# Performance work log

Hardware: AMD Instinct MI355X
Metric: run time of the kernel (lower is better)

Reference implementation:

```python
import jax, jax.numpy as jnp
import numpy as np

N_NODES = 100000
N_EDGES = 1600000
IN_C, HID_C, OUT_C = 64, 64, 16


def _sage_conv(x, src, dst, W_l, b_l, W_r, num_nodes):
    # PyG SAGEConv (aggr='mean'): out = lin_l(mean_{j->i} x_j) + lin_r(x_i)
    # aggregate first (cheap small-d features), then one GEMM
    msg_sum = jax.ops.segment_sum(x[src], dst, num_segments=num_nodes)
    deg = jax.ops.segment_sum(jnp.ones_like(dst, dtype=x.dtype), dst,
                              num_segments=num_nodes)
    mean = msg_sum / jnp.maximum(deg, 1.0)[:, None]
    return mean @ W_l + b_l + x @ W_r


def setup_inputs() -> dict:
    key = jax.random.key(0)
    ks = jax.random.split(key, 8)
    x = jax.random.normal(ks[0], (N_NODES, IN_C), dtype=jnp.float32)
    edge_index = jax.random.randint(ks[1], (2, N_EDGES), 0, N_NODES, dtype=jnp.int64)
    # Glorot-ish init for weights; lin_l has bias, lin_r has none (PyG default)
    def glorot(k, fan_in, fan_out):
        s = jnp.sqrt(6.0 / (fan_in + fan_out))
        return jax.random.uniform(k, (fan_in, fan_out), jnp.float32, -s, s)
    return {
        "x": x,
        "edge_index": edge_index,
        "W1_l": glorot(ks[2], IN_C, HID_C),
        "b1": jnp.zeros((HID_C,), jnp.float32),
        "W1_r": glorot(ks[3], IN_C, HID_C),
        "W2_l": glorot(ks[4], HID_C, OUT_C),
        "b2": jnp.zeros((OUT_C,), jnp.float32),
        "W2_r": glorot(ks[5], HID_C, OUT_C),
    }


def reference(x, edge_index, W1_l, b1, W1_r, W2_l, b2, W2_r):
    src, dst = edge_index[0], edge_index[1]
    h = _sage_conv(x, src, dst, W1_l, b1, W1_r, N_NODES)
    h = jax.nn.relu(h)
    # dropout p=0.3 is identity in eval mode
    out = _sage_conv(h, src, dst, W2_l, b2, W2_r, N_NODES)
    return out
```

## Files before the change

kernel.cpp:

```cpp
#include <hip/hip_runtime.h>
#include <hip/hip_fp16.h>

#define N_NODES 100000
#define N_EDGES 1600000
#define IN_C 64
#define HID_C 64
#define OUT_C 16

#define BKT 256
#define BSH 8
#define NBKT 391
#define CAP 5120
#define GB 512
#define EPB 3125
#define G1B 1563

typedef _Float16 f16x8 __attribute__((ext_vector_type(8)));
typedef float f32x4 __attribute__((ext_vector_type(4)));
typedef float f32x16 __attribute__((ext_vector_type(16)));

__global__ __launch_bounds__(256) void k_merged1(
    const int* __restrict__ src, const int* __restrict__ dst,
    int* __restrict__ gcnt, int* __restrict__ binned,
    const float* __restrict__ x, const float* __restrict__ Wl,
    const float* __restrict__ Wr, const float* __restrict__ b,
    __half* __restrict__ p, __half* __restrict__ q) {
  __shared__ _Float16 sA[64 * 68];
  __shared__ _Float16 sW[128 * 68];
  int t = threadIdx.x;

  if (blockIdx.x < GB) {
    int* h   = (int*)sA;
    int* cur = (int*)sW;
    for (int i = t; i < NBKT; i += 256) h[i] = 0;
    __syncthreads();
    int base = blockIdx.x * EPB;
    int end = base + EPB;
    for (int e = base + t; e < end; e += 256)
      atomicAdd(&h[dst[e] >> BSH], 1);
    __syncthreads();
    for (int i = t; i < NBKT; i += 256) {
      int c = h[i];
      int b0 = atomicAdd(&gcnt[i], c);
      cur[i] = i * CAP + b0;
    }
    __syncthreads();
    for (int e = base + t; e < end; e += 256) {
      int d = dst[e];
      int pos = atomicAdd(&cur[d >> BSH], 1);
      binned[pos] = (src[e] << BSH) | (d & (BKT - 1));
    }
    return;
  }

  int n0 = (blockIdx.x - GB) * 64;

  for (int f = t; f < 1024; f += 256) {
    int r = f >> 4, c4 = f & 15;
    int n = n0 + r;
    float4 v = {0.0f, 0.0f, 0.0f, 0.0f};
    if (n < N_NODES) v = *(const float4*)&x[(size_t)n * 64 + c4 * 4];
    union { _Float16 h[4]; float2 f2; } u;
    u.h[0] = (_Float16)v.x; u.h[1] = (_Float16)v.y;
    u.h[2] = (_Float16)v.z; u.h[3] = (_Float16)v.w;
    *(float2*)&sA[r * 68 + c4 * 4] = u.f2;
  }
  for (int f = t; f < 2048; f += 256) {
    int k = f >> 5, c4 = f & 31;
    float4 w = (c4 < 16) ? *(const float4*)&Wl[k * 64 + c4 * 4]
                         : *(const float4*)&Wr[k * 64 + (c4 - 16) * 4];
    int c = c4 * 4;
    sW[(c + 0) * 68 + k] = (_Float16)w.x;
    sW[(c + 1) * 68 + k] = (_Float16)w.y;
    sW[(c + 2) * 68 + k] = (_Float16)w.z;
    sW[(c + 3) * 68 + k] = (_Float16)w.w;
  }
  __syncthreads();

  int w = t >> 6, lane = t & 63;
  int m = lane & 31, half = lane >> 5;
  int rt = w & 1, cg = w >> 1;

  f32x16 acc[2];
#pragma unroll
  for (int r = 0; r < 16; ++r) { acc[0][r] = 0.0f; acc[1][r] = 0.0f; }

  const _Float16* pA = &sA[(rt * 32 + m) * 68 + half * 8];
  const _Float16* pB0 = &sW[(cg * 64 + m) * 68 + half * 8];
  const _Float16* pB1 = &sW[(cg * 64 + 32 + m) * 68 + half * 8];
#pragma unroll
  for (int kc = 0; kc < 4; ++kc) {
    union { f16x8 v; float2 f2[2]; } a, b0, b1;
    a.f2[0] = *(const float2*)(pA + kc * 16);
    a.f2[1] = *(const float2*)(pA + kc * 16 + 4);
    b0.f2[0] = *(const float2*)(pB0 + kc * 16);
    b0.f2[1] = *(const float2*)(pB0 + kc * 16 + 4);
    b1.f2[0] = *(const float2*)(pB1 + kc * 16);
    b1.f2[1] = *(const float2*)(pB1 + kc * 16 + 4);
    acc[0] = __builtin_amdgcn_mfma_f32_32x32x16_f16(a.v, b0.v, acc[0], 0, 0, 0);
    acc[1] = __builtin_amdgcn_mfma_f32_32x32x16_f16(a.v, b1.v, acc[1], 0, 0, 0);
  }

  if (cg == 0) {
#pragma unroll
    for (int tt = 0; tt < 2; ++tt) {
      int col = tt * 32 + m;
#pragma unroll
      for (int r = 0; r < 16; ++r) {
        int row = (r & 3) + 4 * half + 8 * (r >> 2);
        int n = n0 + rt * 32 + row;
        if (n < N_NODES) p[(size_t)n * 64 + col] = __float2half(acc[tt][r]);
      }
    }
  } else {
    float bias[2] = {b[m], b[32 + m]};
#pragma unroll
    for (int tt = 0; tt < 2; ++tt) {
      int col = tt * 32 + m;
#pragma unroll
      for (int r = 0; r < 16; ++r) {
        int row = (r & 3) + 4 * half + 8 * (r >> 2);
        int n = n0 + rt * 32 + row;
        if (n < N_NODES)
          q[(size_t)n * 64 + col] = __float2half(acc[tt][r] + bias[tt]);
      }
    }
  }
}

__global__ __launch_bounds__(1024) void k_fuse1c(
    const float4* __restrict__ p1, const int* __restrict__ gcnt,
    const int* __restrict__ binned, const float* __restrict__ W2l,
    const float* __restrict__ W2r, const float* __restrict__ b2,
    const float4* __restrict__ q1, int* __restrict__ csr,
    int* __restrict__ rowstart, int* __restrict__ cnt,
    __half* __restrict__ p2, float* __restrict__ q2) {
  __shared__ int hcnt[BKT];
  __shared__ int hscan[BKT];
  __shared__ int cur[BKT];
  __shared__ int lcsr[CAP];
  __shared__ _Float16 sH[256 * 68];
  __shared__ _Float16 sW[32 * 68];
  int b = blockIdx.x;
  int t = threadIdx.x;

  if (t < 512) {
    int k = t >> 3, c4v = t & 7;
    float4 w = (c4v < 4) ? *(const float4*)&W2l[k * 16 + c4v * 4]
                         : *(const float4*)&W2r[k * 16 + (c4v - 4) * 4];
    int c = c4v * 4;
    sW[(c + 0) * 68 + k] = (_Float16)w.x;
    sW[(c + 1) * 68 + k] = (_Float16)w.y;
    sW[(c + 2) * 68 + k] = (_Float16)w.z;
    sW[(c + 3) * 68 + k] = (_Float16)w.w;
  }
  if (t < BKT) hcnt[t] = 0;
  __syncthreads();

  int start = b * CAP;
  int total = gcnt[b];
  for (int i = t; i < total; i += 1024)
    atomicAdd(&hcnt[binned[start + i] & (BKT - 1)], 1);
  __syncthreads();
  int v = 0;
  if (t < BKT) {
    v = hcnt[t];
    hscan[t] = v;
  }
  __syncthreads();
  for (int st = 1; st < 256; st <<= 1) {
    int a = 0;
    if (t < BKT && t >= st) a = hscan[t - st];
    __syncthreads();
    if (t < BKT) hscan[t] += a;
    __syncthreads();
  }
  if (t < BKT) {
    cur[t] = hscan[t] - v;
    int n = (b << BSH) + t;
    if (n < N_NODES) {
      rowstart[n] = start + hscan[t] - v;
      cnt[n] = v;
    }
  }
  __syncthreads();
  for (int i = t; i < total; i += 1024) {
    int vv = binned[start + i];
    int pos = atomicAdd(&cur[vv & (BKT - 1)], 1);
    lcsr[pos] = vv >> BSH;
  }
  __syncthreads();
  for (int i = t; i < total; i += 1024) csr[start + i] = lcsr[i];

  int g = t >> 3, c4 = t & 7;
  for (int r = g; r < BKT; r += 128) {
    int n = (b << BSH) + r;
    if (n >= N_NODES) continue;
    int deg = hcnt[r];
    int row = hscan[r] - deg;
    float acc[8];
#pragma unroll
    for (int m = 0; m < 8; ++m) acc[m] = 0.0f;
    int j = 0;
    for (; j + 8 <= deg; j += 8) {
      int idx[8];
#pragma unroll
      for (int u = 0; u < 8; ++u) idx[u] = lcsr[row + j + u];
      float4 av[8];
#pragma unroll
      for (int u = 0; u < 8; ++u) av[u] = p1[idx[u] * 8 + c4];
#pragma unroll
      for (int u = 0; u < 8; ++u) {
        const __half2* h = (const __half2*)&av[u];
#pragma unroll
        for (int m = 0; m < 4; ++m) {
          float2 f = __half22float2(h[m]);
          acc[2 * m] += f.x;
          acc[2 * m + 1] += f.y;
        }
      }
    }
    for (; j < deg; ++j) {
      float4 a = p1[lcsr[row + j] * 8 + c4];
      const __half2* h = (const __half2*)&a;
#pragma unroll
      for (int m = 0; m < 4; ++m) {
        float2 f = __half22float2(h[m]);
        acc[2 * m] += f.x;
        acc[2 * m + 1] += f.y;
      }
    }
    float inv = 1.0f / fmaxf((float)deg, 1.0f);
    float4 qv = q1[n * 8 + c4];
    __half2* qh = (__half2*)&qv;
    union { __half2 h2[2]; float2 f2; } u01, u23;
#pragma unroll
    for (int m = 0; m < 2; ++m) {
      float2 f = __half22float2(qh[m]);
      float2 s;
      s.x = fmaxf(acc[2 * m] * inv + f.x, 0.0f);
      s.y = fmaxf(acc[2 * m + 1] * inv + f.y, 0.0f);
      u01.h2[m] = __float22half2_rn(s);
    }
#pragma unroll
    for (int m = 2; m < 4; ++m) {
      float2 f = __half22float2(qh[m]);
      float2 s;
      s.x = fmaxf(acc[2 * m] * inv + f.x, 0.0f);
      s.y = fmaxf(acc[2 * m + 1] * inv + f.y, 0.0f);
      u23.h2[m - 2] = __float22half2_rn(s);
    }
    *(float2*)&sH[r * 68 + c4 * 8] = u01.f2;
    *(float2*)&sH[r * 68 + c4 * 8 + 4] = u23.f2;
  }
  __syncthreads();

  int wv = t >> 6, lane = t & 63;
  int n16 = lane & 15, quad = lane >> 4;
  f32x4 aP, aQ;
#pragma unroll
  for (int r = 0; r < 4; ++r) { aP[r] = 0.0f; aQ[r] = 0.0f; }
  const _Float16* pA = &sH[(wv * 16 + n16) * 68 + quad * 8];
  const _Float16* pBP = &sW[n16 * 68 + quad * 8];
  const _Float16* pBQ = &sW[(16 + n16) * 68 + quad * 8];
#pragma unroll
  for (int kc = 0; kc < 2; ++kc) {
    union { f16x8 v; float2 f2[2]; } a, bp, bq;
    a.f2[0] = *(const float2*)(pA + kc * 32);
    a.f2[1] = *(const float2*)(pA + kc * 32 + 4);
    bp.f2[0] = *(const float2*)(pBP + kc * 32);
    bp.f2[1] = *(const float2*)(pBP + kc * 32 + 4);
    bq.f2[0] = *(const float2*)(pBQ + kc * 32);
    bq.f2[1] = *(const float2*)(pBQ + kc * 32 + 4);
    aP = __builtin_amdgcn_mfma_f32_16x16x32_f16(a.v, bp.v, aP, 0, 0, 0);
    aQ = __builtin_amdgcn_mfma_f32_16x16x32_f16(a.v, bq.v, aQ, 0, 0, 0);
  }
  float bias = b2[n16];
#pragma unroll
  for (int r = 0; r < 4; ++r) {
    int row = wv * 16 + quad * 4 + r;
    int n = (b << BSH) + row;
    if (n < N_NODES) {
      p2[(size_t)n * 16 + n16] = __float2half(aP[r]);
      q2[(size_t)n * 16 + n16] = aQ[r] + bias;
    }
  }
}

__global__ __launch_bounds__(256) void k_fuse2(
    const float4* __restrict__ p2, const float4* __restrict__ q2,
    const int* __restrict__ rowstart, const int* __restrict__ cnt,
    const int* __restrict__ csr, float4* __restrict__ out) {
  int t = threadIdx.x;
  int n = blockIdx.x * 128 + (t >> 1);
  if (n >= N_NODES) return;
  int c8 = t & 1;
  int row = rowstart[n];
  int deg = cnt[n];
  float acc[8];
#pragma unroll
  for (int m = 0; m < 8; ++m) acc[m] = 0.0f;
  int j = 0;
  for (; j + 8 <= deg; j += 8) {
    int idx[8];
#pragma unroll
    for (int u = 0; u < 8; ++u) idx[u] = csr[row + j + u];
    float4 av[8];
#pragma unroll
    for (int u = 0; u < 8; ++u) av[u] = p2[idx[u] * 2 + c8];
#pragma unroll
    for (int u = 0; u < 8; ++u) {
      const __half2* h = (const __half2*)&av[u];
#pragma unroll
      for (int m = 0; m < 4; ++m) {
        float2 f = __half22float2(h[m]);
        acc[2 * m] += f.x;
        acc[2 * m + 1] += f.y;
      }
    }
  }
  for (; j < deg; ++j) {
    float4 a = p2[csr[row + j] * 2 + c8];
    const __half2* h = (const __half2*)&a;
#pragma unroll
    for (int m = 0; m < 4; ++m) {
      float2 f = __half22float2(h[m]);
      acc[2 * m] += f.x;
      acc[2 * m + 1] += f.y;
    }
  }
  float inv = 1.0f / fmaxf((float)deg, 1.0f);
  float4 q0 = q2[n * 4 + c8 * 2];
  float4 q1v = q2[n * 4 + c8 * 2 + 1];
  float4 o0 = {acc[0] * inv + q0.x, acc[1] * inv + q0.y,
               acc[2] * inv + q0.z, acc[3] * inv + q0.w};
  float4 o1 = {acc[4] * inv + q1v.x, acc[5] * inv + q1v.y,
               acc[6] * inv + q1v.z, acc[7] * inv + q1v.w};
  out[n * 4 + c8 * 2] = o0;
  out[n * 4 + c8 * 2 + 1] = o1;
}

extern "C" void kernel_launch(void* const* d_in, const int* in_sizes, int n_in,
                              void* d_out, int out_size, void* d_ws, size_t ws_size,
                              hipStream_t stream) {
  const float* x   = (const float*)d_in[0];
  const int* edge  = (const int*)d_in[1];
  const int* src   = edge;
  const int* dst   = edge + N_EDGES;
  const float* W1l = (const float*)d_in[2];
  const float* b1  = (const float*)d_in[3];
  const float* W1r = (const float*)d_in[4];
  const float* W2l = (const float*)d_in[5];
  const float* b2  = (const float*)d_in[6];
  const float* W2r = (const float*)d_in[7];
  float* out = (float*)d_out;

  int* gcnt     = (int*)d_ws;
  int* rowstart = gcnt + 512;
  int* cnt      = rowstart + N_NODES;
  int* binned   = cnt + N_NODES;
  int* csr      = binned + NBKT * CAP;
  __half* p1    = (__half*)(csr + NBKT * CAP);
  __half* q1    = p1 + (size_t)N_NODES * 64;
  __half* p2    = q1 + (size_t)N_NODES * 64;
  float* q2     = (float*)(p2 + (size_t)N_NODES * 16);

  hipMemsetAsync(gcnt, 0, NBKT * sizeof(int), stream);

  k_merged1<<<GB + G1B, 256, 0, stream>>>(src, dst, gcnt, binned,
                                          x, W1l, W1r, b1, p1, q1);
  k_fuse1c<<<NBKT, 1024, 0, stream>>>((const float4*)p1, gcnt, binned,
                                      W2l, W2r, b2, (const float4*)q1,
                                      csr, rowstart, cnt, p2, q2);
  k_fuse2<<<(N_NODES + 127) / 128, 256, 0, stream>>>((const float4*)p2,
                                                     (const float4*)q2,
                                                     rowstart, cnt, csr,
                                                     (float4*)out);
}
```

Measured before the change: 189.0 us.

## Halve bucket size to double fuse1c blocks and split MFMA work across waves

Shrinks destination buckets from 256 to 128 nodes, which doubles the number of k_fuse1c blocks so the 256 CUs have more work. Each thread now aggregates exactly one row, and the P and Q GEMM halves go to different waves instead of one wave doing both. The binning phase preloads src/dst into registers once instead of reading dst twice, and skips global atomics for empty buckets. The cost is more global bucket atomics and per-block setup overhead, plus tighter per-bucket capacity margins (CAP 2560).

```diff
diff --git a/kernel.cpp b/kernel.cpp
--- a/kernel.cpp
+++ b/kernel.cpp
@@ -7,12 +7,13 @@
 #define HID_C 64
 #define OUT_C 16
 
-#define BKT 256
-#define BSH 8
-#define NBKT 391
-#define CAP 5120
+#define BKT 128
+#define BSH 7
+#define NBKT 782
+#define CAP 2560
 #define GB 512
 #define EPB 3125
+#define NIT 13
 #define G1B 1563
 
 typedef _Float16 f16x8 __attribute__((ext_vector_type(8)));
@@ -36,19 +37,31 @@
     __syncthreads();
     int base = blockIdx.x * EPB;
     int end = base + EPB;
-    for (int e = base + t; e < end; e += 256)
-      atomicAdd(&h[dst[e] >> BSH], 1);
+    int dv[NIT], sv[NIT];
+#pragma unroll
+    for (int it = 0; it < NIT; ++it) {
+      int e = base + t + it * 256;
+      bool ok = (e < end);
+      dv[it] = ok ? dst[e] : -1;
+      sv[it] = ok ? src[e] : 0;
+    }
+#pragma unroll
+    for (int it = 0; it < NIT; ++it)
+      if (dv[it] >= 0) atomicAdd(&h[dv[it] >> BSH], 1);
     __syncthreads();
     for (int i = t; i < NBKT; i += 256) {
       int c = h[i];
-      int b0 = atomicAdd(&gcnt[i], c);
+      int b0 = (c > 0) ? atomicAdd(&gcnt[i], c) : 0;
       cur[i] = i * CAP + b0;
     }
     __syncthreads();
-    for (int e = base + t; e < end; e += 256) {
-      int d = dst[e];
-      int pos = atomicAdd(&cur[d >> BSH], 1);
-      binned[pos] = (src[e] << BSH) | (d & (BKT - 1));
+#pragma unroll
+    for (int it = 0; it < NIT; ++it) {
+      if (dv[it] >= 0) {
+        int d = dv[it];
+        int pos = atomicAdd(&cur[d >> BSH], 1);
+        binned[pos] = (sv[it] << BSH) | (d & (BKT - 1));
+      }
     }
     return;
   }
@@ -139,7 +152,7 @@
   __shared__ int hscan[BKT];
   __shared__ int cur[BKT];
   __shared__ int lcsr[CAP];
-  __shared__ _Float16 sH[256 * 68];
+  __shared__ _Float16 sH[128 * 68];
   __shared__ _Float16 sW[32 * 68];
   int b = blockIdx.x;
   int t = threadIdx.x;
@@ -168,7 +181,7 @@
     hscan[t] = v;
   }
   __syncthreads();
-  for (int st = 1; st < 256; st <<= 1) {
+  for (int st = 1; st < BKT; st <<= 1) {
     int a = 0;
     if (t < BKT && t >= st) a = hscan[t - st];
     __syncthreads();
@@ -192,26 +205,37 @@
   __syncthreads();
   for (int i = t; i < total; i += 1024) csr[start + i] = lcsr[i];
 
-  int g = t >> 3, c4 = t & 7;
-  for (int r = g; r < BKT; r += 128) {
+  {
+    int r = t >> 3, c4 = t & 7;
     int n = (b << BSH) + r;
-    if (n >= N_NODES) continue;
-    int deg = hcnt[r];
-    int row = hscan[r] - deg;
-    float acc[8];
-#pragma unroll
-    for (int m = 0; m < 8; ++m) acc[m] = 0.0f;
-    int j = 0;
-    for (; j + 8 <= deg; j += 8) {
-      int idx[8];
-#pragma unroll
-      for (int u = 0; u < 8; ++u) idx[u] = lcsr[row + j + u];
-      float4 av[8];
-#pragma unroll
-      for (int u = 0; u < 8; ++u) av[u] = p1[idx[u] * 8 + c4];
-#pragma unroll
-      for (int u = 0; u < 8; ++u) {
-        const __half2* h = (const __half2*)&av[u];
+    if (n < N_NODES) {
+      int deg = hcnt[r];
+      int row = hscan[r] - deg;
+      float acc[8];
+#pragma unroll
+      for (int m = 0; m < 8; ++m) acc[m] = 0.0f;
+      int j = 0;
+      for (; j + 8 <= deg; j += 8) {
+        int idx[8];
+#pragma unroll
+        for (int u = 0; u < 8; ++u) idx[u] = lcsr[row + j + u];
+        float4 av[8];
+#pragma unroll
+        for (int u = 0; u < 8; ++u) av[u] = p1[idx[u] * 8 + c4];
+#pragma unroll
+        for (int u = 0; u < 8; ++u) {
+          const __half2* h = (const __half2*)&av[u];
+#pragma unroll
+          for (int m = 0; m < 4; ++m) {
+            float2 f = __half22float2(h[m]);
+            acc[2 * m] += f.x;
+            acc[2 * m + 1] += f.y;
+          }
+        }
+      }
+      for (; j < deg; ++j) {
+        float4 a = p1[lcsr[row + j] * 8 + c4];
+        const __half2* h = (const __half2*)&a;
 #pragma unroll
         for (int m = 0; m < 4; ++m) {
           float2 f = __half22float2(h[m]);
@@ -219,70 +243,67 @@
           acc[2 * m + 1] += f.y;
         }
       }
-    }
-    for (; j < deg; ++j) {
-      float4 a = p1[lcsr[row + j] * 8 + c4];
-      const __half2* h = (const __half2*)&a;
-#pragma unroll
-      for (int m = 0; m < 4; ++m) {
-        float2 f = __half22float2(h[m]);
-        acc[2 * m] += f.x;
-        acc[2 * m + 1] += f.y;
-      }
-    }
-    float inv = 1.0f / fmaxf((float)deg, 1.0f);
-    float4 qv = q1[n * 8 + c4];
-    __half2* qh = (__half2*)&qv;
-    union { __half2 h2[2]; float2 f2; } u01, u23;
-#pragma unroll
-    for (int m = 0; m < 2; ++m) {
-      float2 f = __half22float2(qh[m]);
-      float2 s;
-      s.x = fmaxf(acc[2 * m] * inv + f.x, 0.0f);
-      s.y = fmaxf(acc[2 * m + 1] * inv + f.y, 0.0f);
-      u01.h2[m] = __float22half2_rn(s);
-    }
-#pragma unroll
-    for (int m = 2; m < 4; ++m) {
-      float2 f = __half22float2(qh[m]);
-      float2 s;
-      s.x = fmaxf(acc[2 * m] * inv + f.x, 0.0f);
-      s.y = fmaxf(acc[2 * m + 1] * inv + f.y, 0.0f);
-      u23.h2[m - 2] = __float22half2_rn(s);
-    }
-    *(float2*)&sH[r * 68 + c4 * 8] = u01.f2;
-    *(float2*)&sH[r * 68 + c4 * 8 + 4] = u23.f2;
+      float inv = 1.0f / fmaxf((float)deg, 1.0f);
+      float4 qv = q1[n * 8 + c4];
+      __half2* qh = (__half2*)&qv;
+      union { __half2 h2[2]; float2 f2; } u01, u23;
+#pragma unroll
+      for (int m = 0; m < 2; ++m) {
+        float2 f = __half22float2(qh[m]);
+        float2 s;
+        s.x = fmaxf(acc[2 * m] * inv + f.x, 0.0f);
+        s.y = fmaxf(acc[2 * m + 1] * inv + f.y, 0.0f);
+        u01.h2[m] = __float22half2_rn(s);
+      }
+#pragma unroll
+      for (int m = 2; m < 4; ++m) {
+        float2 f = __half22float2(qh[m]);
+        float2 s;
+        s.x = fmaxf(acc[2 * m] * inv + f.x, 0.0f);
+        s.y = fmaxf(acc[2 * m + 1] * inv + f.y, 0.0f);
+        u23.h2[m - 2] = __float22half2_rn(s);
+      }
+      *(float2*)&sH[r * 68 + c4 * 8] = u01.f2;
+      *(float2*)&sH[r * 68 + c4 * 8 + 4] = u23.f2;
+    } else if (r < BKT) {
+      *(float2*)&sH[r * 68 + c4 * 8] = make_float2(0.0f, 0.0f);
+      *(float2*)&sH[r * 68 + c4 * 8 + 4] = make_float2(0.0f, 0.0f);
+    }
   }
   __syncthreads();
 
   int wv = t >> 6, lane = t & 63;
   int n16 = lane & 15, quad = lane >> 4;
-  f32x4 aP, aQ;
-#pragma unroll
-  for (int r = 0; r < 4; ++r) { aP[r] = 0.0f; aQ[r] = 0.0f; }
-  const _Float16* pA = &sH[(wv * 16 + n16) * 68 + quad * 8];
-  const _Float16* pBP = &sW[n16 * 68 + quad * 8];
-  const _Float16* pBQ = &sW[(16 + n16) * 68 + quad * 8];
+  int rt = wv & 7;
+  bool isQ = wv >= 8;
+  f32x4 acc;
+#pragma unroll
+  for (int r = 0; r < 4; ++r) acc[r] = 0.0f;
+  const _Float16* pA = &sH[(rt * 16 + n16) * 68 + quad * 8];
+  const _Float16* pB = &sW[((isQ ? 16 : 0) + n16) * 68 + quad * 8];
 #pragma unroll
   for (int kc = 0; kc < 2; ++kc) {
-    union { f16x8 v; float2 f2[2]; } a, bp, bq;
+    union { f16x8 v; float2 f2[2]; } a, bb;
     a.f2[0] = *(const float2*)(pA + kc * 32);
     a.f2[1] = *(const float2*)(pA + kc * 32 + 4);
-    bp.f2[0] = *(const float2*)(pBP + kc * 32);
-    bp.f2[1] = *(const float2*)(pBP + kc * 32 + 4);
-    bq.f2[0] = *(const float2*)(pBQ + kc * 32);
-    bq.f2[1] = *(const float2*)(pBQ + kc * 32 + 4);
-    aP = __builtin_amdgcn_mfma_f32_16x16x32_f16(a.v, bp.v, aP, 0, 0, 0);
-    aQ = __builtin_amdgcn_mfma_f32_16x16x32_f16(a.v, bq.v, aQ, 0, 0, 0);
-  }
-  float bias = b2[n16];
-#pragma unroll
-  for (int r = 0; r < 4; ++r) {
-    int row = wv * 16 + quad * 4 + r;
-    int n = (b << BSH) + row;
-    if (n < N_NODES) {
-      p2[(size_t)n * 16 + n16] = __float2half(aP[r]);
-      q2[(size_t)n * 16 + n16] = aQ[r] + bias;
+    bb.f2[0] = *(const float2*)(pB + kc * 32);
+    bb.f2[1] = *(const float2*)(pB + kc * 32 + 4);
+    acc = __builtin_amdgcn_mfma_f32_16x16x32_f16(a.v, bb.v, acc, 0, 0, 0);
+  }
+  if (!isQ) {
+#pragma unroll
+    for (int r = 0; r < 4; ++r) {
+      int row = rt * 16 + quad * 4 + r;
+      int n = (b << BSH) + row;
+      if (n < N_NODES) p2[(size_t)n * 16 + n16] = __float2half(acc[r]);
+    }
+  } else {
+    float bias = b2[n16];
+#pragma unroll
+    for (int r = 0; r < 4; ++r) {
+      int row = rt * 16 + quad * 4 + r;
+      int n = (b << BSH) + row;
+      if (n < N_NODES) q2[(size_t)n * 16 + n16] = acc[r] + bias;
     }
   }
 }
@@ -356,7 +377,7 @@
   float* out = (float*)d_out;
 
   int* gcnt     = (int*)d_ws;
-  int* rowstart = gcnt + 512;
+  int* rowstart = gcnt + 1024;
   int* cnt      = rowstart + N_NODES;
   int* binned   = cnt + N_NODES;
   int* csr      = binned + NBKT * CAP;
```

Result: slower. 195.7 us (+3.6%).
